# Kernel tuning notes

Hardware: AMD Instinct MI355X
Metric: run time of the kernel (lower is better)

Reference implementation:

```python
import jax, jax.numpy as jnp
import numpy as np

N_PTS = 200000
N_EDGES = 1600000
REL_W = 7          # 1 tex col + 2 slots of (vx, vy, tex_rt)
MEM_W = 63         # quantization: values in [0, 63]
LIN_RAD = 1.0
N_ROLL = 5
MEM_SIZE = 2 ** 27 # dense emulation of the sparse COO count memory
MASK = (MEM_SIZE // 64) - 1  # for modular base-64 Horner hashing


def setup_inputs() -> dict:
    key = jax.random.key(0)
    k1, k2, k3 = jax.random.split(key, 3)
    pts = jax.random.uniform(k1, (N_PTS, 2), dtype=jnp.float32)
    tex = jax.random.uniform(k2, (N_PTS, 1), dtype=jnp.float32)
    edges = jax.random.randint(k3, (N_EDGES, 2), 0, N_PTS, dtype=jnp.int64)
    mem = jnp.zeros((MEM_SIZE,), dtype=jnp.float32)
    return {"pts": pts, "tex": tex, "edges": edges, "mem": mem}


def _build_rel(pts, tex, edges):
    # filter_thresh: binarize texture at 0.7
    tex_b = (tex[:, 0] > 0.7).astype(jnp.int32)            # [N]
    # symmetrize edge list (frnn returns one direction)
    e = jnp.concatenate([edges, edges[:, ::-1]], axis=0)   # [E, 2]
    src, dst = e[:, 0], e[:, 1]
    # quantized relative displacement vectors
    d = pts[dst] - pts[src]                                # [E, 2]
    vecs = jnp.clip(jnp.round(((d / LIN_RAD) + 1.0) / 2.0 * MEM_W), 0, MEM_W).astype(jnp.int32)
    tex_rt = tex_b[dst]                                    # [E]
    # occurrence rank of each edge within its source row (== write_cols logic)
    E = src.shape[0]
    order = jnp.argsort(src, stable=True)
    sr = src[order]
    idx = jnp.arange(E, dtype=jnp.int32)
    is_start = jnp.concatenate([jnp.array([True]), sr[1:] != sr[:-1]])
    seg_start = jax.lax.associative_scan(jnp.maximum, jnp.where(is_start, idx, 0))
    occ = jnp.zeros(E, jnp.int32).at[order].set(idx - seg_start)
    # only the first (REL_W-1)//3 slots per row fit; others are skipped
    valid = occ < (REL_W - 1) // 3
    col = 1 + 3 * occ
    N = pts.shape[0]
    wrow = jnp.where(valid, src, N)  # out-of-range row -> dropped by scatter
    rel = jnp.zeros((N, REL_W), jnp.int32).at[:, 0].set(tex_b)
    rel = rel.at[wrow, col].set(vecs[:, 0], mode='drop')
    rel = rel.at[wrow, col + 1].set(vecs[:, 1], mode='drop')
    rel = rel.at[wrow, col + 2].set(tex_rt, mode='drop')
    return rel


def _roll_rel(rel, n_roll):
    # home tex (col 0) stays; remaining cols roll by 3*i
    rolled = [jnp.concatenate([rel[:, :1], jnp.roll(rel[:, 1:], 3 * i, axis=1)], axis=1)
              for i in range(n_roll + 1)]
    return jnp.concatenate(rolled, axis=0)


def _hash_rows(rel_all):
    # base-64 Horner hash mod 2^27 (emulates sparse COO multi-index)
    v = jnp.clip(rel_all, 0, MEM_W)  # each column in [0, 63]
    acc = jnp.zeros(rel_all.shape[0], jnp.int32)
    for j in range(REL_W - 1, -1, -1):
        acc = (acc & MASK) * 64 + v[:, j]
    return acc


def reference(pts, tex, edges, mem):
    rel0 = _roll_rel(_build_rel(pts, tex, edges), N_ROLL)
    rel1 = _roll_rel(_build_rel(pts, tex, edges), N_ROLL)
    rel_all = jnp.concatenate([rel0, rel1], axis=0)        # [2*(n_roll+1)*N, REL_W]
    flat = _hash_rows(rel_all)
    # mem.add_(sparse_coo(ones at rel_vec indices)) -> scatter-add count histogram
    return mem.at[flat].add(1.0)
```

## Files before the change

### kernel.cpp

```cpp
#include <hip/hip_runtime.h>

#define N_PTS   200000
#define N_EDGES 1600000
#define MEM_SIZE (1 << 27)

#define COPY_BLOCKS  32768
#define F4_PER_BLOCK 1024

#define NP   25
#define NPB  8192
#define EP   16
#define EPS  (N_EDGES / EP)
#define EPS4 (EPS / 2)
#define SCAN_T 1024

__device__ __forceinline__ void upd2(unsigned* __restrict__ mn1, unsigned* __restrict__ mn2,
                                     int a, unsigned i) {
    if ((unsigned)a < NPB) {
        unsigned old = atomicMin(&mn1[a], i);
        unsigned c = (i < old) ? old : i;
        if (c != 0xFFFFFFFFu) atomicMin(&mn2[a], c);
    }
}

__device__ __forceinline__ void proc(unsigned* __restrict__ mn1, unsigned* __restrict__ mn2,
                                     int lo, int4 p, int g ) {
    unsigned ia0 = (unsigned)(2 * g);
    unsigned ib0 = (unsigned)(2 * g + N_EDGES);
    upd2(mn1, mn2, p.x - lo, ia0);
    upd2(mn1, mn2, p.y - lo, ib0);
    upd2(mn1, mn2, p.z - lo, ia0 + 1u);
    upd2(mn1, mn2, p.w - lo, ib0 + 1u);
}

__global__ __launch_bounds__(SCAN_T) void scan_2min(const int4* __restrict__ edges4,
                                                    unsigned long long* __restrict__ W) {
    __shared__ unsigned mn1[NPB];
    __shared__ unsigned mn2[NPB];

    int b  = blockIdx.x;
    int ep = b / NP;
    int np = b % NP;
    int lo = np * NPB;

    for (int j = threadIdx.x; j < NPB; j += SCAN_T) { mn1[j] = 0xFFFFFFFFu; mn2[j] = 0xFFFFFFFFu; }
    __syncthreads();

    int q0 = ep * EPS4;
    int k = threadIdx.x;
    for (; k + 3 * SCAN_T < EPS4; k += 4 * SCAN_T) {
        int g0 = q0 + k;
        int4 p0 = edges4[g0];
        int4 p1 = edges4[g0 + SCAN_T];
        int4 p2 = edges4[g0 + 2 * SCAN_T];
        int4 p3 = edges4[g0 + 3 * SCAN_T];
        proc(mn1, mn2, lo, p0, g0);
        proc(mn1, mn2, lo, p1, g0 + SCAN_T);
        proc(mn1, mn2, lo, p2, g0 + 2 * SCAN_T);
        proc(mn1, mn2, lo, p3, g0 + 3 * SCAN_T);
    }
    for (; k < EPS4; k += SCAN_T) {
        int g = q0 + k;
        int4 p = edges4[g];
        proc(mn1, mn2, lo, p, g);
    }
    __syncthreads();

    for (int j = threadIdx.x; j < NPB; j += SCAN_T) {
        int n = lo + j;
        if (n < N_PTS)
            W[(size_t)ep * N_PTS + n] =
                ((unsigned long long)mn2[j] << 32) | (unsigned long long)mn1[j];
    }
}

__global__ void copy_mem(const float4* __restrict__ src, float4* __restrict__ dst) {
    int base = blockIdx.x * F4_PER_BLOCK + threadIdx.x;
    float4 v0 = src[base];
    float4 v1 = src[base + 256];
    float4 v2 = src[base + 512];
    float4 v3 = src[base + 768];
    dst[base]       = v0;
    dst[base + 256] = v1;
    dst[base + 512] = v2;
    dst[base + 768] = v3;
}

__device__ __forceinline__ int quant6(float d) {
    float x = ((d + 1.0f) / 2.0f) * 63.0f;
    float r = rintf(x);
    r = fminf(fmaxf(r, 0.0f), 63.0f);
    return (int)r;
}

__global__ void finalize(const float* __restrict__ pts, const float* __restrict__ tex,
                         const int2* __restrict__ edges,
                         const unsigned long long* __restrict__ W,
                         float* __restrict__ out) {
    int n = blockIdx.x * blockDim.x + threadIdx.x;
    if (n >= N_PTS) return;

    unsigned int k1 = 0xFFFFFFFFu, k2 = 0xFFFFFFFFu;
    #pragma unroll
    for (int s = 0; s < EP; ++s) {
        unsigned long long pr = W[(size_t)s * N_PTS + n];
        unsigned int m1 = (unsigned int)(pr & 0xFFFFFFFFu);
        unsigned int m2 = (unsigned int)(pr >> 32);
        if (m1 < k1) { k2 = k1; k1 = m1; } else if (m1 < k2) { k2 = m1; }
        if (m2 < k2 && m2 > k1) { k2 = m2; }
    }

    float px = pts[2 * n], py = pts[2 * n + 1];
    int t = (tex[n] > 0.7f) ? 1 : 0;

    int v0x = 0, v0y = 0, t0 = 0, v1x = 0, v1y = 0, t1 = 0;

    if (k1 < 2u * N_EDGES) {
        int k = (int)k1;
        int2 e = edges[(k < N_EDGES) ? k : (k - N_EDGES)];
        int dst = (k < N_EDGES) ? e.y : e.x;
        v0x = quant6(pts[2 * dst] - px);
        v0y = quant6(pts[2 * dst + 1] - py);
        t0 = (tex[dst] > 0.7f) ? 1 : 0;
    }
    if (k2 < 2u * N_EDGES) {
        int k = (int)k2;
        int2 e = edges[(k < N_EDGES) ? k : (k - N_EDGES)];
        int dst = (k < N_EDGES) ? e.y : e.x;
        v1x = quant6(pts[2 * dst] - px);
        v1y = quant6(pts[2 * dst + 1] - py);
        t1 = (tex[dst] > 0.7f) ? 1 : 0;
    }

    int h_id = t | (v0x << 6) | (v0y << 12) | (t0 << 18) | ((v1x & 7) << 24);
    int h_sw = t | (v1x << 6) | (v1y << 12) | (t1 << 18) | ((v0x & 7) << 24);

    atomicAdd(&out[h_id], 6.0f);
    atomicAdd(&out[h_sw], 6.0f);
}

extern "C" void kernel_launch(void* const* d_in, const int* in_sizes, int n_in,
                              void* d_out, int out_size, void* d_ws, size_t ws_size,
                              hipStream_t stream) {
    const float* pts   = (const float*)d_in[0];
    const float* tex   = (const float*)d_in[1];
    const int2*  edges = (const int2*)d_in[2];
    const float* mem   = (const float*)d_in[3];
    float*       out   = (float*)d_out;

    unsigned long long* W = (unsigned long long*)d_ws;

    scan_2min<<<NP * EP, SCAN_T, 0, stream>>>((const int4*)edges, W);
    copy_mem<<<COPY_BLOCKS, 256, 0, stream>>>((const float4*)mem, (float4*)out);
    finalize<<<(N_PTS + 255) / 256, 256, 0, stream>>>(pts, tex, edges, W, out);
}
```

Baseline: 273.1 us.

## Fuse memory copy into edge scan kernel to overlap bandwidth and LDS atomics

Merges the 512 MB mem-to-out copy into the scan kernel, so each block interleaves copy loads and stores with edge loads and shared-memory atomic min updates. The point partition changes to 32 slices of 6400 points, giving 512 blocks and a grid-stride copy loop. The aim is to hide the LDS atomic work behind the memory-bound copy and drop one kernel launch. In exchange, only 512 blocks drive the copy, which may limit achieved bandwidth, and it no longer uses the earlier many-block copy layout.

```diff
diff --git a/kernel.cpp b/kernel.cpp
--- a/kernel.cpp
+++ b/kernel.cpp
@@ -4,15 +4,17 @@
 #define N_EDGES 1600000
 #define MEM_SIZE (1 << 27)
 
-#define COPY_BLOCKS  32768
-#define F4_PER_BLOCK 1024
-
-#define NP   25
-#define NPB  8192
+#define NP   32
+#define NPB  6400
 #define EP   16
 #define EPS  (N_EDGES / EP)
 #define EPS4 (EPS / 2)
-#define SCAN_T 1024
+#define NBLK (NP * EP)
+#define NTHR 1024
+#define NF4  (MEM_SIZE / 4)
+#define CSTRIDE (NBLK * NTHR)
+#define CITER (NF4 / CSTRIDE)
+#define SITER ((EPS4 + NTHR - 1) / NTHR)
 
 __device__ __forceinline__ void upd2(unsigned* __restrict__ mn1, unsigned* __restrict__ mn2,
                                      int a, unsigned i) {
@@ -33,57 +35,44 @@
     upd2(mn1, mn2, p.w - lo, ib0 + 1u);
 }
 
-__global__ __launch_bounds__(SCAN_T) void scan_2min(const int4* __restrict__ edges4,
-                                                    unsigned long long* __restrict__ W) {
+__global__ __launch_bounds__(NTHR) void fused_copy_scan(const float4* __restrict__ src,
+                                                        float4* __restrict__ dst,
+                                                        const int4* __restrict__ edges4,
+                                                        unsigned long long* __restrict__ W) {
     __shared__ unsigned mn1[NPB];
     __shared__ unsigned mn2[NPB];
 
     int b  = blockIdx.x;
-    int ep = b / NP;
-    int np = b % NP;
+    int ep = b >> 5;
+    int np = b & 31;
     int lo = np * NPB;
+    int t  = threadIdx.x;
 
-    for (int j = threadIdx.x; j < NPB; j += SCAN_T) { mn1[j] = 0xFFFFFFFFu; mn2[j] = 0xFFFFFFFFu; }
+    for (int j = t; j < NPB; j += NTHR) { mn1[j] = 0xFFFFFFFFu; mn2[j] = 0xFFFFFFFFu; }
     __syncthreads();
 
     int q0 = ep * EPS4;
-    int k = threadIdx.x;
-    for (; k + 3 * SCAN_T < EPS4; k += 4 * SCAN_T) {
-        int g0 = q0 + k;
-        int4 p0 = edges4[g0];
-        int4 p1 = edges4[g0 + SCAN_T];
-        int4 p2 = edges4[g0 + 2 * SCAN_T];
-        int4 p3 = edges4[g0 + 3 * SCAN_T];
-        proc(mn1, mn2, lo, p0, g0);
-        proc(mn1, mn2, lo, p1, g0 + SCAN_T);
-        proc(mn1, mn2, lo, p2, g0 + 2 * SCAN_T);
-        proc(mn1, mn2, lo, p3, g0 + 3 * SCAN_T);
-    }
-    for (; k < EPS4; k += SCAN_T) {
-        int g = q0 + k;
-        int4 p = edges4[g];
-        proc(mn1, mn2, lo, p, g);
+    int cbase = b * NTHR + t;
+
+    #pragma unroll 4
+    for (int j = 0; j < CITER; ++j) {
+        int ci = cbase + j * CSTRIDE;
+        float4 v = src[ci];
+        int k = t + j * NTHR;
+        bool have = (j < SITER) && (k < EPS4);
+        int4 p;
+        if (have) p = edges4[q0 + k];
+        dst[ci] = v;
+        if (have) proc(mn1, mn2, lo, p, q0 + k);
     }
     __syncthreads();
 
-    for (int j = threadIdx.x; j < NPB; j += SCAN_T) {
+    for (int j = t; j < NPB; j += NTHR) {
         int n = lo + j;
         if (n < N_PTS)
             W[(size_t)ep * N_PTS + n] =
                 ((unsigned long long)mn2[j] << 32) | (unsigned long long)mn1[j];
     }
-}
-
-__global__ void copy_mem(const float4* __restrict__ src, float4* __restrict__ dst) {
-    int base = blockIdx.x * F4_PER_BLOCK + threadIdx.x;
-    float4 v0 = src[base];
-    float4 v1 = src[base + 256];
-    float4 v2 = src[base + 512];
-    float4 v3 = src[base + 768];
-    dst[base]       = v0;
-    dst[base + 256] = v1;
-    dst[base + 512] = v2;
-    dst[base + 768] = v3;
 }
 
 __device__ __forceinline__ int quant6(float d) {
@@ -150,7 +139,7 @@
 
     unsigned long long* W = (unsigned long long*)d_ws;
 
-    scan_2min<<<NP * EP, SCAN_T, 0, stream>>>((const int4*)edges, W);
-    copy_mem<<<COPY_BLOCKS, 256, 0, stream>>>((const float4*)mem, (float4*)out);
+    fused_copy_scan<<<NBLK, NTHR, 0, stream>>>(
+        (const float4*)mem, (float4*)out, (const int4*)edges, W);
     finalize<<<(N_PTS + 255) / 256, 256, 0, stream>>>(pts, tex, edges, W, out);
 }
```

New measurement: 261.3 us. -4.3%, faster.
